# Kernel optimization log

Measured on AMD Instinct MI355X. Metric: run time of the kernel, lower is better.

## Reference

```python
import jax, jax.numpy as jnp
import numpy as np

B = 262144
EDGES_SRC = np.array([0, 0, 0, 0])
EDGES_DST = np.array([1, 2, 3, 4])
PRED_IDS = np.array([[0, 10, 14], [1, 11, 18], [2, 12, 22], [3, 13, 26]])
O_IDS = np.array([0, 1, 2, 3, 10, 11, 12, 13, 14, 18, 22, 26])


def _xavier(k, shape):
    fan_out, fan_in = shape
    bound = float(np.sqrt(6.0 / (fan_in + fan_out)))
    return jax.random.uniform(k, shape, jnp.float32, -bound, bound)


def setup_inputs() -> dict:
    key = jax.random.key(0)
    ks = jax.random.split(key, 12)
    return {
        "initial_c": jax.random.uniform(ks[0], (B, 30), jnp.float32),
        "initial_s": jax.random.normal(ks[1], (B, 9), jnp.float32),
        "current_c": jax.random.uniform(ks[2], (B, 30), jnp.float32),
        "eps": jax.random.normal(ks[3], (B, 8), jnp.float32),
        # GnnMessagePassing params (torch Linear: y = x @ W.T + b)
        "W1": _xavier(ks[4], (128, 13)), "b1": jnp.zeros(128, jnp.float32),
        "W2": _xavier(ks[5], (39, 128)), "b2": jnp.zeros(39, jnp.float32),
        "W3": _xavier(ks[6], (128, 39)), "b3": jnp.zeros(128, jnp.float32),
        "Wm": _xavier(ks[7], (8, 128)), "bm": jnp.zeros(8, jnp.float32),
        "Wv": _xavier(ks[8], (8, 128)), "bv": jnp.zeros(8, jnp.float32),
        # Decoder params: [25 -> 32 -> 12], sigmoid output (binary=True)
        "Wd1": _xavier(ks[9], (32, 25)), "bd1": jnp.zeros(32, jnp.float32),
        "Wd2": _xavier(ks[10], (12, 32)), "bd2": jnp.zeros(12, jnp.float32),
    }


def reference(initial_c, initial_s, current_c, eps,
              W1, b1, W2, b2, W3, b3, Wm, bm, Wv, bv, Wd1, bd1, Wd2, bd2):
    bsz = current_c.shape[0]
    eye = jnp.eye(5, dtype=current_c.dtype)
    # per-edge constant one-hot pair features: [4, 10]
    edge_onehot = jnp.concatenate([eye[EDGES_SRC], eye[EDGES_DST]], axis=-1)
    edge_onehot = jnp.broadcast_to(edge_onehot[:, None, :], (4, bsz, 10))
    # gather predicate triplets per edge: [B, 4, 3] -> [4, B, 3]
    preds = jnp.transpose(current_c[:, PRED_IDS], (1, 0, 2))
    inp_mp = jnp.concatenate([edge_onehot, preds], axis=-1)  # [4, B, 13]

    # message MLP + sum over edge dim
    x = jax.nn.relu(jnp.einsum('ebi,oi->ebo', inp_mp, W1) + b1)  # [4, B, 128]
    x = jax.nn.relu(jnp.einsum('ebi,oi->ebo', x, W2) + b2)       # [4, B, 39]
    x = x.sum(axis=0)                                            # [B, 39]
    x = jax.nn.relu(x @ W3.T + b3)                               # [B, 128]
    means = x @ Wm.T + bm                                        # [B, 8]
    log_var = x @ Wv.T + bv                                      # [B, 8]

    # reparameterization
    z = eps * jnp.exp(0.5 * log_var) + means

    # decoder: [one-hot(node 0) | initial_c[o_ids] | z] -> sigmoid MLP
    node0 = jnp.broadcast_to(eye[0], (bsz, 5))
    inp_dec = jnp.concatenate([node0, initial_c[:, O_IDS], z], axis=1)  # [B, 25]
    h = jax.nn.relu(inp_dec @ Wd1.T + bd1)
    recon_x = jax.nn.sigmoid(h @ Wd2.T + bd2)  # [B, 12]
    return recon_x, means, log_var, z
```

## Files before the change

### kernel.cpp

```cpp
#include <hip/hip_runtime.h>
#include <hip/hip_bf16.h>

#define TPB 256

typedef __attribute__((ext_vector_type(8))) short short8;
typedef __attribute__((ext_vector_type(4))) float f32x4;

#define G_W2F   0
#define G_MVF   12288
#define G_D1F   16384
#define G_D2F   18432
#define G_CEAB  19456
#define G_B2P   23552
#define G_B3    23744
#define G_BMV   24256
#define G_D1C   24320
#define G_BD2   24448
#define G_LCOPY 24512
#define G_W3F   24512
#define G_END   40896

#define PW_SZ   6912
#define PW_SWC  0
#define PW_SIC  768
#define PW_ST   1792
#define PW_X3T  1792
#define PW_MLV  5888
#define PW_HT   5888
#define LDS_TOT (G_LCOPY + 4 * PW_SZ)

__device__ __forceinline__ unsigned short f2bf(float f) {
    unsigned int u = __float_as_uint(f);
    unsigned int r = u + 0x7fffu + ((u >> 16) & 1u);
    return (unsigned short)(r >> 16);
}
__device__ __forceinline__ float lo16(unsigned int d) { return __uint_as_float(d << 16); }
__device__ __forceinline__ float hi16(unsigned int d) { return __uint_as_float(d & 0xffff0000u); }
__device__ __forceinline__ unsigned int pk(float a, float b) {
    __hip_bfloat162 h = __float22bfloat162_rn(make_float2(a, b));
    unsigned int u; __builtin_memcpy(&u, &h, 4); return u;
}
__device__ __forceinline__ unsigned short bfbits(float v) {
    return (unsigned short)(pk(v, v) & 0xffffu);
}

__global__ void prep_kernel(
    const float* __restrict__ W1, const float* __restrict__ b1,
    const float* __restrict__ W2, const float* __restrict__ b2,
    const float* __restrict__ W3, const float* __restrict__ b3,
    const float* __restrict__ Wm, const float* __restrict__ bm,
    const float* __restrict__ Wv, const float* __restrict__ bv,
    const float* __restrict__ Wd1, const float* __restrict__ bd1,
    const float* __restrict__ Wd2, const float* __restrict__ bd2,
    unsigned char* __restrict__ ws)
{
    const int t0 = threadIdx.x;
    unsigned short* w2f = (unsigned short*)(ws + G_W2F);
    for (int i = t0; i < 6144; i += TPB) {
        int j = i & 7, lane = (i >> 3) & 63, ts = i >> 9;
        int tt = ts >> 2, s = ts & 3;
        int n = 16 * tt + (lane & 15), k = 32 * s + 8 * (lane >> 4) + j;
        w2f[i] = (n < 39) ? f2bf(W2[n * 128 + k]) : 0;
    }
    unsigned short* w3f = (unsigned short*)(ws + G_W3F);
    for (int i = t0; i < 8192; i += TPB) {
        int j = i & 7, lane = (i >> 3) & 63, ns = i >> 9;
        int nt = ns >> 1, s = ns & 1;
        int n = 16 * nt + (lane & 15), k = 32 * s + 8 * (lane >> 4) + j;
        w3f[i] = (k < 39) ? f2bf(W3[n * 39 + k]) : 0;
    }
    unsigned short* mvf = (unsigned short*)(ws + G_MVF);
    for (int i = t0; i < 2048; i += TPB) {
        int j = i & 7, lane = (i >> 3) & 63, s = i >> 9;
        int n = lane & 15, k = 32 * s + 8 * (lane >> 4) + j;
        mvf[i] = f2bf(n < 8 ? Wm[n * 128 + k] : Wv[(n - 8) * 128 + k]);
    }
    unsigned short* d1f = (unsigned short*)(ws + G_D1F);
    for (int i = t0; i < 1024; i += TPB) {
        int j = i & 7, lane = (i >> 3) & 63, tt = i >> 9;
        int n = 16 * tt + (lane & 15), k = 8 * (lane >> 4) + j;
        d1f[i] = (k < 20) ? f2bf(Wd1[n * 25 + 5 + k]) : 0;
    }
    unsigned short* d2f = (unsigned short*)(ws + G_D2F);
    for (int i = t0; i < 512; i += TPB) {
        int j = i & 7, lane = i >> 3;
        int n = lane & 15, k = 8 * (lane >> 4) + j;
        d2f[i] = (n < 12) ? f2bf(Wd2[n * 32 + k]) : 0;
    }
    unsigned short* ceab = (unsigned short*)(ws + G_CEAB);
    for (int i = t0; i < 2048; i += TPB) {
        int c = i & 3, o = (i >> 2) & 127, e = i >> 9;
        float v = (c == 0) ? (W1[o * 13 + 0] + W1[o * 13 + 6 + e] + b1[o])
                           : W1[o * 13 + 9 + c];
        ceab[i] = f2bf(v);
    }
    float* fb = (float*)(ws + G_B2P);
    for (int i = t0; i < 48; i += TPB) fb[i] = (i < 39) ? b2[i] : 0.f;
    fb = (float*)(ws + G_B3);
    for (int i = t0; i < 128; i += TPB) fb[i] = b3[i];
    fb = (float*)(ws + G_BMV);
    for (int i = t0; i < 16; i += TPB) fb[i] = (i < 8) ? bm[i] : bv[i - 8];
    fb = (float*)(ws + G_D1C);
    for (int i = t0; i < 32; i += TPB) fb[i] = Wd1[i * 25 + 0] + bd1[i];
    fb = (float*)(ws + G_BD2);
    for (int i = t0; i < 16; i += TPB) fb[i] = (i < 12) ? bd2[i] : 0.f;
}

union S8 { short8 v; uint4 u; };

__global__ __launch_bounds__(TPB, 2) void vae_mfma(
    const float* __restrict__ ic, const float* __restrict__ cc,
    const float* __restrict__ eps,
    const unsigned char* __restrict__ ws,
    float* __restrict__ out, int B)
{
    __shared__ __attribute__((aligned(16))) unsigned char lds[LDS_TOT];
    const int tid = threadIdx.x;

    {
        const uint4* src = (const uint4*)ws;
        uint4* dst = (uint4*)lds;
        #pragma unroll
        for (int it = 0; it < 6; it++) {
            int idx = it * TPB + tid;
            if (idx < G_LCOPY / 16) dst[idx] = src[idx];
        }
    }
    __syncthreads();

    const int lane = tid & 63, w = tid >> 6;
    const int quad = lane >> 4, n16 = lane & 15;
    const long rb = ((long)blockIdx.x * 4 + w) * 16;
    unsigned char* pw = lds + G_LCOPY + w * PW_SZ;

    {
        int r = lane >> 2, g = lane & 3;
        long R = rb + r;
        const int cbase[4] = {0, 2, 10, 12};
        const int csing[4] = {14, 18, 22, 26};
        const float* crow = cc + R * 30;
        const float* irow = ic + R * 30;
        float2 cp = *(const float2*)(crow + cbase[g]);
        float  cs = crow[csing[g]];
        float2 ip = *(const float2*)(irow + cbase[g]);
        float  is = irow[csing[g]];
        float* swc = (float*)(pw + PW_SWC);
        *(float2*)(swc + r * 12 + 2 * g) = cp;
        swc[r * 12 + 8 + g] = cs;
        unsigned short* sic = (unsigned short*)(pw + PW_SIC);
        *(unsigned int*)(sic + r * 32 + 2 * g) = pk(ip.x, ip.y);
        sic[r * 32 + 8 + g] = bfbits(is);
        if (g < 3) *(unsigned long long*)(sic + r * 32 + 20 + 4 * g) = 0ull;
        unsigned short* st = (unsigned short*)(pw + PW_ST);
        *(unsigned long long*)(st + r * 64 + 48 + 4 * g) = 0ull;
    }

    short8 B2[12];
    #pragma unroll
    for (int ts = 0; ts < 12; ts++) {
        S8 x; x.u = *(const uint4*)(lds + G_W2F + (ts * 64 + lane) * 16);
        B2[ts] = x.v;
    }
    const float b2v0 = *(const float*)(lds + G_B2P + n16 * 4);
    const float b2v1 = *(const float*)(lds + G_B2P + (16 + n16) * 4);
    const float b2v2 = *(const float*)(lds + G_B2P + (32 + n16) * 4);

    f32x4 ss0 = {0,0,0,0}, ss1 = {0,0,0,0}, ss2 = {0,0,0,0};
    const float* swc = (const float*)(pw + PW_SWC);

    #pragma unroll
    for (int e = 0; e < 4; e++) {
        float p0 = swc[n16 * 12 + e];
        float p1 = swc[n16 * 12 + 4 + e];
        float p2 = swc[n16 * 12 + 8 + e];
        f32x4 c0 = {b2v0, b2v0, b2v0, b2v0};
        f32x4 c1 = {b2v1, b2v1, b2v1, b2v1};
        f32x4 c2 = {b2v2, b2v2, b2v2, b2v2};
        #pragma unroll
        for (int s = 0; s < 4; s++) {
            const uint4* cea = (const uint4*)(lds + G_CEAB + (e * 128 + s * 32 + quad * 8) * 8);
            float xf[8];
            #pragma unroll
            for (int u = 0; u < 4; u++) {
                uint4 q = cea[u];
                float t = lo16(q.x);
                t = fmaf(hi16(q.x), p0, t);
                t = fmaf(lo16(q.y), p1, t);
                t = fmaf(hi16(q.y), p2, t);
                xf[2 * u] = fmaxf(t, 0.f);
                t = lo16(q.z);
                t = fmaf(hi16(q.z), p0, t);
                t = fmaf(lo16(q.w), p1, t);
                t = fmaf(hi16(q.w), p2, t);
                xf[2 * u + 1] = fmaxf(t, 0.f);
            }
            S8 a;
            a.u.x = pk(xf[0], xf[1]); a.u.y = pk(xf[2], xf[3]);
            a.u.z = pk(xf[4], xf[5]); a.u.w = pk(xf[6], xf[7]);
            c0 = __builtin_amdgcn_mfma_f32_16x16x32_bf16(a.v, B2[s],     c0, 0, 0, 0);
            c1 = __builtin_amdgcn_mfma_f32_16x16x32_bf16(a.v, B2[4 + s], c1, 0, 0, 0);
            c2 = __builtin_amdgcn_mfma_f32_16x16x32_bf16(a.v, B2[8 + s], c2, 0, 0, 0);
        }
        #pragma unroll
        for (int r = 0; r < 4; r++) {
            ss0[r] += fmaxf(c0[r], 0.f);
            ss1[r] += fmaxf(c1[r], 0.f);
            ss2[r] += fmaxf(c2[r], 0.f);
        }
    }

    unsigned short* st = (unsigned short*)(pw + PW_ST);
    #pragma unroll
    for (int r = 0; r < 4; r++) {
        int row = quad * 4 + r;
        st[row * 64 + n16]      = bfbits(ss0[r]);
        st[row * 64 + 16 + n16] = bfbits(ss1[r]);
        st[row * 64 + 32 + n16] = bfbits(ss2[r]);
    }

    S8 A30, A31;
    A30.u = *(const uint4*)(st + n16 * 64 + quad * 8);
    A31.u = *(const uint4*)(st + n16 * 64 + 32 + quad * 8);
    const uint4* w3g = (const uint4*)(ws + G_W3F);
    unsigned short* x3t = (unsigned short*)(pw + PW_X3T);
    const float* b3p = (const float*)(lds + G_B3);
    #pragma unroll
    for (int nt = 0; nt < 8; nt++) {
        float bb = b3p[nt * 16 + n16];
        f32x4 c = {bb, bb, bb, bb};
        S8 bf0, bf1;
        bf0.u = w3g[(nt * 2 + 0) * 64 + lane];
        bf1.u = w3g[(nt * 2 + 1) * 64 + lane];
        c = __builtin_amdgcn_mfma_f32_16x16x32_bf16(A30.v, bf0.v, c, 0, 0, 0);
        c = __builtin_amdgcn_mfma_f32_16x16x32_bf16(A31.v, bf1.v, c, 0, 0, 0);
        #pragma unroll
        for (int r = 0; r < 4; r++)
            x3t[(quad * 4 + r) * 128 + nt * 16 + n16] = bfbits(fmaxf(c[r], 0.f));
    }

    S8 Ah0, Ah1, Ah2, Ah3;
    Ah0.u = *(const uint4*)(x3t + n16 * 128 + 0  + quad * 8);
    Ah1.u = *(const uint4*)(x3t + n16 * 128 + 32 + quad * 8);
    Ah2.u = *(const uint4*)(x3t + n16 * 128 + 64 + quad * 8);
    Ah3.u = *(const uint4*)(x3t + n16 * 128 + 96 + quad * 8);
    float bmvv = *(const float*)(lds + G_BMV + n16 * 4);
    f32x4 cm = {bmvv, bmvv, bmvv, bmvv};
    {
        S8 bm0; bm0.u = *(const uint4*)(lds + G_MVF + (0 * 64 + lane) * 16);
        cm = __builtin_amdgcn_mfma_f32_16x16x32_bf16(Ah0.v, bm0.v, cm, 0, 0, 0);
        S8 bm1; bm1.u = *(const uint4*)(lds + G_MVF + (1 * 64 + lane) * 16);
        cm = __builtin_amdgcn_mfma_f32_16x16x32_bf16(Ah1.v, bm1.v, cm, 0, 0, 0);
        S8 bm2; bm2.u = *(const uint4*)(lds + G_MVF + (2 * 64 + lane) * 16);
        cm = __builtin_amdgcn_mfma_f32_16x16x32_bf16(Ah2.v, bm2.v, cm, 0, 0, 0);
        S8 bm3; bm3.u = *(const uint4*)(lds + G_MVF + (3 * 64 + lane) * 16);
        cm = __builtin_amdgcn_mfma_f32_16x16x32_bf16(Ah3.v, bm3.v, cm, 0, 0, 0);
    }
    float* mlv = (float*)(pw + PW_MLV);
    #pragma unroll
    for (int r = 0; r < 4; r++) mlv[(quad * 4 + r) * 16 + n16] = cm[r];

    {
        int r = lane >> 2, q2 = (lane & 3) * 2;
        long R = rb + r;
        const float* mrow = mlv + r * 16;
        float2 mn = *(const float2*)(mrow + q2);
        float2 lv = *(const float2*)(mrow + 8 + q2);
        float2 ev = *(const float2*)(eps + R * 8 + q2);
        float z0 = fmaf(ev.x, __expf(0.5f * lv.x), mn.x);
        float z1 = fmaf(ev.y, __expf(0.5f * lv.y), mn.y);
        *(float2*)(out + (long)B * 12 + R * 8 + q2) = mn;
        *(float2*)(out + (long)B * 20 + R * 8 + q2) = lv;
        *(float2*)(out + (long)B * 28 + R * 8 + q2) = make_float2(z0, z1);
        unsigned short* sic = (unsigned short*)(pw + PW_SIC);
        *(unsigned int*)(sic + r * 32 + 12 + q2) = pk(z0, z1);
    }

    S8 Ad;
    Ad.u = *(const uint4*)((const unsigned short*)(pw + PW_SIC) + n16 * 32 + quad * 8);
    unsigned short* ht = (unsigned short*)(pw + PW_HT);
    #pragma unroll
    for (int t = 0; t < 2; t++) {
        float dc = *(const float*)(lds + G_D1C + (t * 16 + n16) * 4);
        f32x4 c = {dc, dc, dc, dc};
        S8 bd; bd.u = *(const uint4*)(lds + G_D1F + (t * 64 + lane) * 16);
        c = __builtin_amdgcn_mfma_f32_16x16x32_bf16(Ad.v, bd.v, c, 0, 0, 0);
        #pragma unroll
        for (int r = 0; r < 4; r++)
            ht[(quad * 4 + r) * 32 + t * 16 + n16] = bfbits(fmaxf(c[r], 0.f));
    }

    S8 Ah2d; Ah2d.u = *(const uint4*)(ht + n16 * 32 + quad * 8);
    float bd2v = *(const float*)(lds + G_BD2 + n16 * 4);
    f32x4 cr = {bd2v, bd2v, bd2v, bd2v};
    S8 b2d; b2d.u = *(const uint4*)(lds + G_D2F + lane * 16);
    cr = __builtin_amdgcn_mfma_f32_16x16x32_bf16(Ah2d.v, b2d.v, cr, 0, 0, 0);
    if (n16 < 12) {
        #pragma unroll
        for (int r = 0; r < 4; r++)
            out[(rb + quad * 4 + r) * 12 + n16] = 1.f / (1.f + __expf(-cr[r]));
    }
}

extern "C" void kernel_launch(void* const* d_in, const int* in_sizes, int n_in,
                              void* d_out, int out_size, void* d_ws, size_t ws_size,
                              hipStream_t stream) {
    const float* ic  = (const float*)d_in[0];
    const float* cc  = (const float*)d_in[2];
    const float* eps = (const float*)d_in[3];

    const int B = in_sizes[3] / 8;
    const int nblocks = B / 64;

    prep_kernel<<<1, TPB, 0, stream>>>(
        (const float*)d_in[4],  (const float*)d_in[5],
        (const float*)d_in[6],  (const float*)d_in[7],
        (const float*)d_in[8],  (const float*)d_in[9],
        (const float*)d_in[10], (const float*)d_in[11],
        (const float*)d_in[12], (const float*)d_in[13],
        (const float*)d_in[14], (const float*)d_in[15],
        (const float*)d_in[16], (const float*)d_in[17],
        (unsigned char*)d_ws);
    vae_mfma<<<nblocks, TPB, 0, stream>>>(
        ic, cc, eps, (const unsigned char*)d_ws, (float*)d_out, B);
}
```

Measured before the change: 202.7 us.

## Compute first MLP layer with MFMA, pad LDS strides, parallelize prep kernel

The first message-MLP layer (3 predicates plus a constant term, 128 outputs) is now computed with 8 zero-padded MFMA ops per edge instead of scalar FMAs on every lane. The result is staged through an LDS buffer and reloaded as A operands for the second layer. LDS row strides are padded (40/72/136/18) to reduce bank conflicts, and the weight-prep kernel now runs across 64 blocks instead of 1. The change trades VALU work for mostly-empty MFMAs plus extra LDS traffic, and raises per-wave LDS use, which may lower occupancy.

```diff
diff --git a/kernel.cpp b/kernel.cpp
--- a/kernel.cpp
+++ b/kernel.cpp
@@ -2,6 +2,7 @@
 #include <hip/hip_bf16.h>
 
 #define TPB 256
+#define PREP_BLOCKS 64
 
 typedef __attribute__((ext_vector_type(8))) short short8;
 typedef __attribute__((ext_vector_type(4))) float f32x4;
@@ -20,13 +21,12 @@
 #define G_W3F   24512
 #define G_END   40896
 
-#define PW_SZ   6912
 #define PW_SWC  0
 #define PW_SIC  768
-#define PW_ST   1792
-#define PW_X3T  1792
-#define PW_MLV  5888
-#define PW_HT   5888
+#define PW_ST   2048
+#define PW_BUF  4352
+#define PW_MH   8704
+#define PW_SZ   9984
 #define LDS_TOT (G_LCOPY + 4 * PW_SZ)
 
 __device__ __forceinline__ unsigned short f2bf(float f) {
@@ -34,8 +34,6 @@
     unsigned int r = u + 0x7fffu + ((u >> 16) & 1u);
     return (unsigned short)(r >> 16);
 }
-__device__ __forceinline__ float lo16(unsigned int d) { return __uint_as_float(d << 16); }
-__device__ __forceinline__ float hi16(unsigned int d) { return __uint_as_float(d & 0xffff0000u); }
 __device__ __forceinline__ unsigned int pk(float a, float b) {
     __hip_bfloat162 h = __float22bfloat162_rn(make_float2(a, b));
     unsigned int u; __builtin_memcpy(&u, &h, 4); return u;
@@ -54,56 +52,57 @@
     const float* __restrict__ Wd2, const float* __restrict__ bd2,
     unsigned char* __restrict__ ws)
 {
-    const int t0 = threadIdx.x;
+    const int g0 = blockIdx.x * TPB + threadIdx.x;
+    const int gs = gridDim.x * TPB;
     unsigned short* w2f = (unsigned short*)(ws + G_W2F);
-    for (int i = t0; i < 6144; i += TPB) {
+    for (int i = g0; i < 6144; i += gs) {
         int j = i & 7, lane = (i >> 3) & 63, ts = i >> 9;
         int tt = ts >> 2, s = ts & 3;
         int n = 16 * tt + (lane & 15), k = 32 * s + 8 * (lane >> 4) + j;
         w2f[i] = (n < 39) ? f2bf(W2[n * 128 + k]) : 0;
     }
     unsigned short* w3f = (unsigned short*)(ws + G_W3F);
-    for (int i = t0; i < 8192; i += TPB) {
+    for (int i = g0; i < 8192; i += gs) {
         int j = i & 7, lane = (i >> 3) & 63, ns = i >> 9;
         int nt = ns >> 1, s = ns & 1;
         int n = 16 * nt + (lane & 15), k = 32 * s + 8 * (lane >> 4) + j;
         w3f[i] = (k < 39) ? f2bf(W3[n * 39 + k]) : 0;
     }
     unsigned short* mvf = (unsigned short*)(ws + G_MVF);
-    for (int i = t0; i < 2048; i += TPB) {
+    for (int i = g0; i < 2048; i += gs) {
         int j = i & 7, lane = (i >> 3) & 63, s = i >> 9;
         int n = lane & 15, k = 32 * s + 8 * (lane >> 4) + j;
         mvf[i] = f2bf(n < 8 ? Wm[n * 128 + k] : Wv[(n - 8) * 128 + k]);
     }
     unsigned short* d1f = (unsigned short*)(ws + G_D1F);
-    for (int i = t0; i < 1024; i += TPB) {
+    for (int i = g0; i < 1024; i += gs) {
         int j = i & 7, lane = (i >> 3) & 63, tt = i >> 9;
         int n = 16 * tt + (lane & 15), k = 8 * (lane >> 4) + j;
         d1f[i] = (k < 20) ? f2bf(Wd1[n * 25 + 5 + k]) : 0;
     }
     unsigned short* d2f = (unsigned short*)(ws + G_D2F);
-    for (int i = t0; i < 512; i += TPB) {
+    for (int i = g0; i < 512; i += gs) {
         int j = i & 7, lane = i >> 3;
         int n = lane & 15, k = 8 * (lane >> 4) + j;
         d2f[i] = (n < 12) ? f2bf(Wd2[n * 32 + k]) : 0;
     }
     unsigned short* ceab = (unsigned short*)(ws + G_CEAB);
-    for (int i = t0; i < 2048; i += TPB) {
-        int c = i & 3, o = (i >> 2) & 127, e = i >> 9;
-        float v = (c == 0) ? (W1[o * 13 + 0] + W1[o * 13 + 6 + e] + b1[o])
-                           : W1[o * 13 + 9 + c];
+    for (int i = g0; i < 2048; i += gs) {
+        int c = i & 3, n = (i >> 2) & 127, e = i >> 9;
+        float v = (c < 3) ? W1[n * 13 + 10 + c]
+                          : (W1[n * 13 + 0] + W1[n * 13 + 6 + e] + b1[n]);
         ceab[i] = f2bf(v);
     }
     float* fb = (float*)(ws + G_B2P);
-    for (int i = t0; i < 48; i += TPB) fb[i] = (i < 39) ? b2[i] : 0.f;
+    for (int i = g0; i < 48; i += gs) fb[i] = (i < 39) ? b2[i] : 0.f;
     fb = (float*)(ws + G_B3);
-    for (int i = t0; i < 128; i += TPB) fb[i] = b3[i];
+    for (int i = g0; i < 128; i += gs) fb[i] = b3[i];
     fb = (float*)(ws + G_BMV);
-    for (int i = t0; i < 16; i += TPB) fb[i] = (i < 8) ? bm[i] : bv[i - 8];
+    for (int i = g0; i < 16; i += gs) fb[i] = (i < 8) ? bm[i] : bv[i - 8];
     fb = (float*)(ws + G_D1C);
-    for (int i = t0; i < 32; i += TPB) fb[i] = Wd1[i * 25 + 0] + bd1[i];
+    for (int i = g0; i < 32; i += gs) fb[i] = Wd1[i * 25 + 0] + bd1[i];
     fb = (float*)(ws + G_BD2);
-    for (int i = t0; i < 16; i += TPB) fb[i] = (i < 12) ? bd2[i] : 0.f;
+    for (int i = g0; i < 16; i += gs) fb[i] = (i < 12) ? bd2[i] : 0.f;
 }
 
 union S8 { short8 v; uint4 u; };
@@ -130,6 +129,7 @@
 
     const int lane = tid & 63, w = tid >> 6;
     const int quad = lane >> 4, n16 = lane & 15;
+    const bool q0 = (quad == 0);
     const long rb = ((long)blockIdx.x * 4 + w) * 16;
     unsigned char* pw = lds + G_LCOPY + w * PW_SZ;
 
@@ -148,11 +148,11 @@
         *(float2*)(swc + r * 12 + 2 * g) = cp;
         swc[r * 12 + 8 + g] = cs;
         unsigned short* sic = (unsigned short*)(pw + PW_SIC);
-        *(unsigned int*)(sic + r * 32 + 2 * g) = pk(ip.x, ip.y);
-        sic[r * 32 + 8 + g] = bfbits(is);
-        if (g < 3) *(unsigned long long*)(sic + r * 32 + 20 + 4 * g) = 0ull;
+        *(unsigned int*)(sic + r * 40 + 2 * g) = pk(ip.x, ip.y);
+        sic[r * 40 + 8 + g] = bfbits(is);
+        if (g < 3) *(unsigned long long*)(sic + r * 40 + 20 + 4 * g) = 0ull;
         unsigned short* st = (unsigned short*)(pw + PW_ST);
-        *(unsigned long long*)(st + r * 64 + 48 + 4 * g) = 0ull;
+        *(unsigned long long*)(st + r * 72 + 48 + 4 * g) = 0ull;
     }
 
     short8 B2[12];
@@ -165,41 +165,54 @@
     const float b2v1 = *(const float*)(lds + G_B2P + (16 + n16) * 4);
     const float b2v2 = *(const float*)(lds + G_B2P + (32 + n16) * 4);
 
+    float pa[4], pb[4], pc[4];
+    {
+        const float* swcr = (const float*)(pw + PW_SWC) + n16 * 12;
+        float4 t0 = *(const float4*)(swcr);
+        float4 t1 = *(const float4*)(swcr + 4);
+        float4 t2 = *(const float4*)(swcr + 8);
+        pa[0] = t0.x; pa[1] = t0.y; pa[2] = t0.z; pa[3] = t0.w;
+        pb[0] = t1.x; pb[1] = t1.y; pb[2] = t1.z; pb[3] = t1.w;
+        pc[0] = t2.x; pc[1] = t2.y; pc[2] = t2.z; pc[3] = t2.w;
+    }
+
     f32x4 ss0 = {0,0,0,0}, ss1 = {0,0,0,0}, ss2 = {0,0,0,0};
-    const float* swc = (const float*)(pw + PW_SWC);
+    unsigned short* x1t = (unsigned short*)(pw + PW_BUF);
 
     #pragma unroll
     for (int e = 0; e < 4; e++) {
-        float p0 = swc[n16 * 12 + e];
-        float p1 = swc[n16 * 12 + 4 + e];
-        float p2 = swc[n16 * 12 + 8 + e];
+        S8 a1;
+        a1.u.x = q0 ? pk(pa[e], pb[e]) : 0u;
+        a1.u.y = q0 ? pk(pc[e], 1.0f) : 0u;
+        a1.u.z = 0u; a1.u.w = 0u;
+        const unsigned long long* cb =
+            (const unsigned long long*)(lds + G_CEAB + e * 1024);
+        f32x4 cr[8];
+        #pragma unroll
+        for (int nt = 0; nt < 8; nt++) {
+            unsigned long long bw = cb[nt * 16 + n16];
+            S8 bf;
+            bf.u.x = q0 ? (unsigned int)bw : 0u;
+            bf.u.y = q0 ? (unsigned int)(bw >> 32) : 0u;
+            bf.u.z = 0u; bf.u.w = 0u;
+            f32x4 z = {0, 0, 0, 0};
+            cr[nt] = __builtin_amdgcn_mfma_f32_16x16x32_bf16(a1.v, bf.v, z, 0, 0, 0);
+        }
+        #pragma unroll
+        for (int nt = 0; nt < 8; nt++) {
+            #pragma unroll
+            for (int r = 0; r < 4; r++)
+                x1t[(quad * 4 + r) * 136 + nt * 16 + n16] = bfbits(fmaxf(cr[nt][r], 0.f));
+        }
         f32x4 c0 = {b2v0, b2v0, b2v0, b2v0};
         f32x4 c1 = {b2v1, b2v1, b2v1, b2v1};
         f32x4 c2 = {b2v2, b2v2, b2v2, b2v2};
         #pragma unroll
         for (int s = 0; s < 4; s++) {
-            const uint4* cea = (const uint4*)(lds + G_CEAB + (e * 128 + s * 32 + quad * 8) * 8);
-            float xf[8];
-            #pragma unroll
-            for (int u = 0; u < 4; u++) {
-                uint4 q = cea[u];
-                float t = lo16(q.x);
-                t = fmaf(hi16(q.x), p0, t);
-                t = fmaf(lo16(q.y), p1, t);
-                t = fmaf(hi16(q.y), p2, t);
-                xf[2 * u] = fmaxf(t, 0.f);
-                t = lo16(q.z);
-                t = fmaf(hi16(q.z), p0, t);
-                t = fmaf(lo16(q.w), p1, t);
-                t = fmaf(hi16(q.w), p2, t);
-                xf[2 * u + 1] = fmaxf(t, 0.f);
-            }
-            S8 a;
-            a.u.x = pk(xf[0], xf[1]); a.u.y = pk(xf[2], xf[3]);
-            a.u.z = pk(xf[4], xf[5]); a.u.w = pk(xf[6], xf[7]);
-            c0 = __builtin_amdgcn_mfma_f32_16x16x32_bf16(a.v, B2[s],     c0, 0, 0, 0);
-            c1 = __builtin_amdgcn_mfma_f32_16x16x32_bf16(a.v, B2[4 + s], c1, 0, 0, 0);
-            c2 = __builtin_amdgcn_mfma_f32_16x16x32_bf16(a.v, B2[8 + s], c2, 0, 0, 0);
+            S8 a2; a2.u = *(const uint4*)(x1t + n16 * 136 + s * 32 + quad * 8);
+            c0 = __builtin_amdgcn_mfma_f32_16x16x32_bf16(a2.v, B2[s],     c0, 0, 0, 0);
+            c1 = __builtin_amdgcn_mfma_f32_16x16x32_bf16(a2.v, B2[4 + s], c1, 0, 0, 0);
+            c2 = __builtin_amdgcn_mfma_f32_16x16x32_bf16(a2.v, B2[8 + s], c2, 0, 0, 0);
         }
         #pragma unroll
         for (int r = 0; r < 4; r++) {
@@ -213,16 +226,16 @@
     #pragma unroll
     for (int r = 0; r < 4; r++) {
         int row = quad * 4 + r;
-        st[row * 64 + n16]      = bfbits(ss0[r]);
-        st[row * 64 + 16 + n16] = bfbits(ss1[r]);
-        st[row * 64 + 32 + n16] = bfbits(ss2[r]);
+        st[row * 72 + n16]      = bfbits(ss0[r]);
+        st[row * 72 + 16 + n16] = bfbits(ss1[r]);
+        st[row * 72 + 32 + n16] = bfbits(ss2[r]);
     }
 
     S8 A30, A31;
-    A30.u = *(const uint4*)(st + n16 * 64 + quad * 8);
-    A31.u = *(const uint4*)(st + n16 * 64 + 32 + quad * 8);
+    A30.u = *(const uint4*)(st + n16 * 72 + quad * 8);
+    A31.u = *(const uint4*)(st + n16 * 72 + 32 + quad * 8);
     const uint4* w3g = (const uint4*)(ws + G_W3F);
-    unsigned short* x3t = (unsigned short*)(pw + PW_X3T);
+    unsigned short* x3t = (unsigned short*)(pw + PW_BUF);
     const float* b3p = (const float*)(lds + G_B3);
     #pragma unroll
     for (int nt = 0; nt < 8; nt++) {
@@ -235,14 +248,14 @@
         c = __builtin_amdgcn_mfma_f32_16x16x32_bf16(A31.v, bf1.v, c, 0, 0, 0);
         #pragma unroll
         for (int r = 0; r < 4; r++)
-            x3t[(quad * 4 + r) * 128 + nt * 16 + n16] = bfbits(fmaxf(c[r], 0.f));
+            x3t[(quad * 4 + r) * 136 + nt * 16 + n16] = bfbits(fmaxf(c[r], 0.f));
     }
 
     S8 Ah0, Ah1, Ah2, Ah3;
-    Ah0.u = *(const uint4*)(x3t + n16 * 128 + 0  + quad * 8);
-    Ah1.u = *(const uint4*)(x3t + n16 * 128 + 32 + quad * 8);
-    Ah2.u = *(const uint4*)(x3t + n16 * 128 + 64 + quad * 8);
-    Ah3.u = *(const uint4*)(x3t + n16 * 128 + 96 + quad * 8);
+    Ah0.u = *(const uint4*)(x3t + n16 * 136 + 0  + quad * 8);
+    Ah1.u = *(const uint4*)(x3t + n16 * 136 + 32 + quad * 8);
+    Ah2.u = *(const uint4*)(x3t + n16 * 136 + 64 + quad * 8);
+    Ah3.u = *(const uint4*)(x3t + n16 * 136 + 96 + quad * 8);
     float bmvv = *(const float*)(lds + G_BMV + n16 * 4);
     f32x4 cm = {bmvv, bmvv, bmvv, bmvv};
     {
@@ -255,29 +268,29 @@
         S8 bm3; bm3.u = *(const uint4*)(lds + G_MVF + (3 * 64 + lane) * 16);
         cm = __builtin_amdgcn_mfma_f32_16x16x32_bf16(Ah3.v, bm3.v, cm, 0, 0, 0);
     }
-    float* mlv = (float*)(pw + PW_MLV);
-    #pragma unroll
-    for (int r = 0; r < 4; r++) mlv[(quad * 4 + r) * 16 + n16] = cm[r];
-
-    {
-        int r = lane >> 2, q2 = (lane & 3) * 2;
+    float* mlv = (float*)(pw + PW_MH);
+    #pragma unroll
+    for (int r = 0; r < 4; r++) mlv[(quad * 4 + r) * 18 + n16] = cm[r];
+
+    {
+        int r = lane >> 2, g = lane & 3;
         long R = rb + r;
-        const float* mrow = mlv + r * 16;
-        float2 mn = *(const float2*)(mrow + q2);
-        float2 lv = *(const float2*)(mrow + 8 + q2);
-        float2 ev = *(const float2*)(eps + R * 8 + q2);
+        const float* mrow = mlv + r * 18;
+        float2 mn = *(const float2*)(mrow + 2 * g);
+        float2 lv = *(const float2*)(mrow + 8 + 2 * g);
+        float2 ev = *(const float2*)(eps + R * 8 + 2 * g);
         float z0 = fmaf(ev.x, __expf(0.5f * lv.x), mn.x);
         float z1 = fmaf(ev.y, __expf(0.5f * lv.y), mn.y);
-        *(float2*)(out + (long)B * 12 + R * 8 + q2) = mn;
-        *(float2*)(out + (long)B * 20 + R * 8 + q2) = lv;
-        *(float2*)(out + (long)B * 28 + R * 8 + q2) = make_float2(z0, z1);
+        *(float2*)(out + (long)B * 12 + R * 8 + 2 * g) = mn;
+        *(float2*)(out + (long)B * 20 + R * 8 + 2 * g) = lv;
+        *(float2*)(out + (long)B * 28 + R * 8 + 2 * g) = make_float2(z0, z1);
         unsigned short* sic = (unsigned short*)(pw + PW_SIC);
-        *(unsigned int*)(sic + r * 32 + 12 + q2) = pk(z0, z1);
+        *(unsigned int*)(sic + r * 40 + 12 + 2 * g) = pk(z0, z1);
     }
 
     S8 Ad;
-    Ad.u = *(const uint4*)((const unsigned short*)(pw + PW_SIC) + n16 * 32 + quad * 8);
-    unsigned short* ht = (unsigned short*)(pw + PW_HT);
+    Ad.u = *(const uint4*)((const unsigned short*)(pw + PW_SIC) + n16 * 40 + quad * 8);
+    unsigned short* ht = (unsigned short*)(pw + PW_MH);
     #pragma unroll
     for (int t = 0; t < 2; t++) {
         float dc = *(const float*)(lds + G_D1C + (t * 16 + n16) * 4);
@@ -286,18 +299,18 @@
         c = __builtin_amdgcn_mfma_f32_16x16x32_bf16(Ad.v, bd.v, c, 0, 0, 0);
         #pragma unroll
         for (int r = 0; r < 4; r++)
-            ht[(quad * 4 + r) * 32 + t * 16 + n16] = bfbits(fmaxf(c[r], 0.f));
-    }
-
-    S8 Ah2d; Ah2d.u = *(const uint4*)(ht + n16 * 32 + quad * 8);
+            ht[(quad * 4 + r) * 40 + t * 16 + n16] = bfbits(fmaxf(c[r], 0.f));
+    }
+
+    S8 Ah2d; Ah2d.u = *(const uint4*)(ht + n16 * 40 + quad * 8);
     float bd2v = *(const float*)(lds + G_BD2 + n16 * 4);
-    f32x4 cr = {bd2v, bd2v, bd2v, bd2v};
+    f32x4 cr2 = {bd2v, bd2v, bd2v, bd2v};
     S8 b2d; b2d.u = *(const uint4*)(lds + G_D2F + lane * 16);
-    cr = __builtin_amdgcn_mfma_f32_16x16x32_bf16(Ah2d.v, b2d.v, cr, 0, 0, 0);
+    cr2 = __builtin_amdgcn_mfma_f32_16x16x32_bf16(Ah2d.v, b2d.v, cr2, 0, 0, 0);
     if (n16 < 12) {
         #pragma unroll
         for (int r = 0; r < 4; r++)
-            out[(rb + quad * 4 + r) * 12 + n16] = 1.f / (1.f + __expf(-cr[r]));
+            out[(rb + quad * 4 + r) * 12 + n16] = 1.f / (1.f + __expf(-cr2[r]));
     }
 }
 
@@ -311,7 +324,7 @@
     const int B = in_sizes[3] / 8;
     const int nblocks = B / 64;
 
-    prep_kernel<<<1, TPB, 0, stream>>>(
+    prep_kernel<<<PREP_BLOCKS, TPB, 0, stream>>>(
         (const float*)d_in[4],  (const float*)d_in[5],
         (const float*)d_in[6],  (const float*)d_in[7],
         (const float*)d_in[8],  (const float*)d_in[9],
```

Result: faster. 195.4 us (-3.6%).
